# Optimization experiments

Measured on AMD Instinct MI355X. Metric: run time of the kernel, lower is better.

The kernel has to match this reference:

```python
import jax, jax.numpy as jnp
from jax import lax
import numpy as np

# torch.sign(torch.sign(x) + 0.5): maps x<0 -> -1, x>=0 -> +1 (zeros go to +1)
def binarize(x):
    return jnp.where(x >= 0, 1.0, -1.0).astype(x.dtype)


def setup_inputs() -> dict:
    key = jax.random.key(0)
    kx, kw, kb = jax.random.split(key, 3)
    x = jax.random.normal(kx, (32, 256, 56, 56), dtype=jnp.float32)
    weight = jax.random.normal(kw, (256, 256, 3, 3), dtype=jnp.float32)
    bias = jax.random.normal(kb, (256,), dtype=jnp.float32)
    return {"x": x, "weight": weight, "bias": bias}


def reference(x, weight, bias):
    b_weight = binarize(weight)  # [O, I, kH, kW] in {-1, +1}
    b_bias = binarize(bias)      # [O] in {-1, +1}
    out = lax.conv_general_dilated(
        x, b_weight,
        window_strides=(1, 1),
        padding=((1, 1), (1, 1)),
        rhs_dilation=(1, 1),
        feature_group_count=1,
        dimension_numbers=("NCHW", "OIHW", "NCHW"),
    )
    return out + b_bias[None, :, None, None]
```

## Files before the change

kernel.cpp:

```cpp
#include <hip/hip_runtime.h>
#include <stdint.h>


#define N_IMG 32
#define C_IN  256
#define H_IN  56
#define W_IN  56
#define O_OUT 256
#define HW    (H_IN * W_IN)
#define K_RAW (C_IN * 9)

typedef int8_t i8x16 __attribute__((ext_vector_type(16)));
typedef int    i32x4 __attribute__((ext_vector_type(4)));
typedef float  f32x4 __attribute__((ext_vector_type(4)));
typedef float  f32x4u __attribute__((ext_vector_type(4), aligned(4)));
typedef __bf16 bf16x8 __attribute__((ext_vector_type(8)));

#define XQ_WSTR (58 * 64)
#define XQ_CSTR (58 * 58 * 64)
#define XQ_BYTES ((size_t)N_IMG * 4 * XQ_CSTR)
#define WQ_BYTES ((size_t)36 * 256 * 64)
#define AM_OFF   (XQ_BYTES + WQ_BYTES)
#define ARR_OFF  (AM_OFF + 64)
#define WS_NEED  (ARR_OFF + 4096)

#define BPITCH  80
#define BS_ROWB (58 * BPITCH)
#define CHUNK_B (3 * 8192)

#define AMAX_BLOCKS 1024

#define AS1 __attribute__((address_space(1)))
#define AS3 __attribute__((address_space(3)))

__device__ __forceinline__ void dma16(const void* g, void* l) {
    __builtin_amdgcn_global_load_lds((const AS1 uint32_t*)g, (AS3 uint32_t*)l, 16, 0, 0);
}

__global__ void prep_combo(const float* __restrict__ x, const float* __restrict__ w,
                           int8_t* __restrict__ wq, float* __restrict__ am_arr) {
    __shared__ __attribute__((aligned(16))) int8_t S[9 * 64 * 64];
    const int bx = blockIdx.x;
    const int t  = threadIdx.x;

    if (bx >= 16) {
        const int b = bx - 16;
        const size_t NV = (size_t)N_IMG * C_IN * HW / 4;
        float m = 0.f;
        for (size_t i = (size_t)b * 256 + t; i < NV; i += (size_t)AMAX_BLOCKS * 256) {
            f32x4 v = ((const f32x4*)x)[i];
            m = fmaxf(m, fmaxf(fmaxf(fabsf(v[0]), fabsf(v[1])),
                               fmaxf(fabsf(v[2]), fabsf(v[3]))));
        }
#pragma unroll
        for (int off = 32; off; off >>= 1)
            m = fmaxf(m, __shfl_down(m, off));
        float* red = (float*)S;
        if ((t & 63) == 0) red[t >> 6] = m;
        __syncthreads();
        if (t == 0)
            am_arr[b] = fmaxf(fmaxf(red[0], red[1]), fmaxf(red[2], red[3]));
        return;
    }

    const int og = bx >> 2;
    const int cc = bx & 3;
    const int o0 = og * 64;
#pragma unroll
    for (int kk = 0; kk < 4; ++kk) {
        const int p   = kk * 256 + t;
        const int o_l = p >> 4;
        const int chg = p & 15;
        const float* src = w + (size_t)(o0 + o_l) * K_RAW + (size_t)(cc * 64 + chg * 4) * 9;
        f32x4u v[9];
#pragma unroll
        for (int q = 0; q < 9; ++q) v[q] = *(const f32x4u*)(src + q * 4);
#pragma unroll
        for (int tap = 0; tap < 9; ++tap) {
            unsigned dw = 0;
#pragma unroll
            for (int co = 0; co < 4; ++co) {
                const int flat = co * 9 + tap;
                const float fv = v[flat >> 2][flat & 3];
                dw |= (unsigned)((fv >= 0.f) ? 0x01u : 0xffu) << (co * 8);
            }
            *(unsigned*)&S[tap * 4096 + o_l * 64 + chg * 4] = dw;
        }
    }
    __syncthreads();
#pragma unroll
    for (int kk = 0; kk < 9; ++kk) {
        const int c    = kk * 256 + t;
        const int tap  = c >> 8;
        const int rem  = c & 255;
        const int o_l  = rem >> 2;
        const int cpos = rem & 3;
        const int truec = (cpos - ((o_l & 15) >> 1)) & 3;
        i32x4 vv = *(const i32x4*)&S[tap * 4096 + o_l * 64 + truec * 16];
        *(i32x4*)(wq + ((size_t)(cc * 9 + tap) * 256 + (o0 + o_l)) * 64 + cpos * 16) = vv;
    }
}

__global__ void xtrans_q(const float* __restrict__ x, int8_t* __restrict__ xq,
                         const float* __restrict__ am_arr,
                         unsigned* __restrict__ am_bits) {
    __shared__ float red[4];
    const int t = threadIdx.x;
    float m = fmaxf(fmaxf(am_arr[t], am_arr[t + 256]),
                    fmaxf(am_arr[t + 512], am_arr[t + 768]));
#pragma unroll
    for (int off = 32; off; off >>= 1)
        m = fmaxf(m, __shfl_down(m, off));
    if ((t & 63) == 0) red[t >> 6] = m;
    __syncthreads();
    m = fmaxf(fmaxf(red[0], red[1]), fmaxf(red[2], red[3]));

    const int bx = blockIdx.x;
    const int cc = blockIdx.y;
    const int n  = blockIdx.z;
    if (bx == 0 && cc == 0 && n == 0 && t == 0) *am_bits = __float_as_uint(m);

    int8_t* plane = xq + (size_t)(n * 4 + cc) * XQ_CSTR;
    if (bx >= 56) {
        const int hh = (bx == 56) ? 0 : 57;
        if (t < 232) *(i32x4*)(plane + (size_t)hh * XQ_WSTR + t * 16) = (i32x4){0, 0, 0, 0};
        return;
    }
    const int hh = bx + 1;
    const int wg = t & 15;
    const int cg = t >> 4;
    int8_t* orow = plane + (size_t)hh * XQ_WSTR;

    if (wg >= 14) {
        const int ww = (wg == 14) ? 0 : 57;
        *(int*)(orow + ww * 64 + cg * 4) = 0;
        return;
    }

    const float scale = 127.f / fmaxf(m, 1e-20f);
    const float* src = x + ((size_t)n * C_IN + cc * 64 + cg * 4) * HW
                         + (size_t)bx * W_IN + wg * 4;
    int8_t qb[4][4];
#pragma unroll
    for (int j = 0; j < 4; ++j) {
        f32x4 v = *(const f32x4*)(src + (size_t)j * HW);
#pragma unroll
        for (int k = 0; k < 4; ++k) {
            float f = v[k] * scale;
            f = fminf(fmaxf(f, -127.f), 127.f);
            qb[j][k] = (int8_t)(int)rintf(f);
        }
    }
#pragma unroll
    for (int k = 0; k < 4; ++k) {
        int d = (int)(uint8_t)qb[0][k] | ((int)(uint8_t)qb[1][k] << 8)
              | ((int)(uint8_t)qb[2][k] << 16) | ((int)(uint8_t)qb[3][k] << 24);
        *(int*)(orow + (wg * 4 + k + 1) * 64 + cg * 4) = d;
    }
}

__launch_bounds__(256, 2)
__global__ void bconv_i8(const int8_t* __restrict__ xq,
                         const int8_t* __restrict__ wq,
                         const float* __restrict__ bias,
                         const unsigned* __restrict__ amax_bits,
                         float* __restrict__ out) {
    __shared__ __attribute__((aligned(16))) int8_t As[2 * CHUNK_B];
    __shared__ __attribute__((aligned(16))) int8_t Bs[6 * BS_ROWB];

    const int tid  = threadIdx.x;
    const int lane = tid & 63;
    const int wv   = tid >> 6;
    const int row  = lane & 15;
    const int quad = lane >> 4;

    const int nrp  = blockIdx.x;
    const int n    = nrp / 14;
    const int rp   = nrp - n * 14;
    const int oblk = blockIdx.y;
    const int h0   = rp * 4;

    int pr[4], pc[4];
    bool live[4];
#pragma unroll
    for (int nt = 0; nt < 4; ++nt) {
        int p = wv * 64 + nt * 16 + row;
        live[nt] = (p < 224);
        int r = p / 56;
        int c = p - r * 56;
        if (!live[nt]) { r = 0; c = 0; }
        pr[nt] = r;
        pc[nt] = c;
    }

    i32x4 acc[8][4];
#pragma unroll
    for (int mt = 0; mt < 8; ++mt)
#pragma unroll
        for (int nt = 0; nt < 4; ++nt)
            acc[mt][nt] = (i32x4){0, 0, 0, 0};

    const int rowA = row * 64 + (((quad + (row >> 1)) & 3) << 4);
    int addrB[4];
#pragma unroll
    for (int nt = 0; nt < 4; ++nt)
        addrB[nt] = pr[nt] * BS_ROWB + pc[nt] * BPITCH + quad * 16;

    auto issueA3 = [&](int c) {
        const int8_t* g = wq + (size_t)(3 * c) * 16384 + oblk * 8192 + wv * 2048 + lane * 16;
        int8_t* l = &As[(c & 1) * CHUNK_B + wv * 2048];
#pragma unroll
        for (int u = 0; u < 3; ++u) {
            dma16(g + u * 16384,        l + u * 8192);
            dma16(g + u * 16384 + 1024, l + u * 8192 + 1024);
        }
    };

    issueA3(0);

    i32x4 af[8], bc[4], bn[4];

    for (int cc = 0; cc < 4; ++cc) {
        __syncthreads();
        if (tid < 232) {
            const int8_t* bbase = xq + (size_t)(n * 4 + cc) * XQ_CSTR
                                     + (size_t)h0 * XQ_WSTR + tid * 16;
            int8_t* ldst = &Bs[(tid >> 2) * BPITCH + (tid & 3) * 16];
            i32x4 hv[6];
#pragma unroll
            for (int r6 = 0; r6 < 6; ++r6)
                hv[r6] = *(const i32x4*)(bbase + r6 * XQ_WSTR);
#pragma unroll
            for (int r6 = 0; r6 < 6; ++r6)
                *(i32x4*)(ldst + r6 * BS_ROWB) = hv[r6];
        }
        __syncthreads();

#pragma unroll
        for (int k = 0; k < 3; ++k) {
            const int c = cc * 3 + k;
            if (k == 0) {
                if (c + 1 < 12) issueA3(c + 1);
#pragma unroll
                for (int nt = 0; nt < 4; ++nt)
                    bc[nt] = *(const i32x4*)(&Bs[addrB[nt]]);
            } else {
                __syncthreads();
                if (c + 1 < 12) issueA3(c + 1);
#pragma unroll
                for (int nt = 0; nt < 4; ++nt) bc[nt] = bn[nt];
            }
            const int8_t* Acur = &As[(c & 1) * CHUNK_B];
#pragma unroll
            for (int mt = 0; mt < 8; ++mt)
                af[mt] = *(const i32x4*)(Acur + mt * 1024 + rowA);

#pragma unroll
            for (int u = 0; u < 3; ++u) {
                if (u < 2) {
                    const int offn = k * BS_ROWB + (u + 1) * BPITCH;
#pragma unroll
                    for (int nt = 0; nt < 4; ++nt)
                        bn[nt] = *(const i32x4*)(&Bs[addrB[nt] + offn]);
                    const int8_t* Anx = Acur + (u + 1) * 8192;
#pragma unroll
                    for (int mt = 0; mt < 8; ++mt) {
                        i32x4 a = af[mt];
#pragma unroll
                        for (int nt = 0; nt < 4; ++nt)
                            acc[mt][nt] = __builtin_amdgcn_mfma_i32_16x16x64_i8(
                                a, bc[nt], acc[mt][nt], 0, 0, 0);
                        af[mt] = *(const i32x4*)(Anx + mt * 1024 + rowA);
                    }
#pragma unroll
                    for (int nt = 0; nt < 4; ++nt) bc[nt] = bn[nt];
                } else {
                    if (k < 2) {
                        const int offn = (k + 1) * BS_ROWB;
#pragma unroll
                        for (int nt = 0; nt < 4; ++nt)
                            bn[nt] = *(const i32x4*)(&Bs[addrB[nt] + offn]);
                    }
#pragma unroll
                    for (int mt = 0; mt < 8; ++mt)
#pragma unroll
                        for (int nt = 0; nt < 4; ++nt)
                            acc[mt][nt] = __builtin_amdgcn_mfma_i32_16x16x64_i8(
                                af[mt], bc[nt], acc[mt][nt], 0, 0, 0);
                }
            }
        }
    }

    const float am  = __uint_as_float(*amax_bits);
    const float inv = am * (1.0f / 127.0f);
    float* base0 = out + ((size_t)n * O_OUT + oblk * 128) * HW;
    int pixoff[4];
#pragma unroll
    for (int nt = 0; nt < 4; ++nt)
        pixoff[nt] = (h0 + pr[nt]) * W_IN + pc[nt];
#pragma unroll
    for (int mt = 0; mt < 8; ++mt) {
        f32x4 bv = *(const f32x4*)(bias + oblk * 128 + mt * 16 + quad * 4);
#pragma unroll
        for (int r = 0; r < 4; ++r) {
            const float sb = (bv[r] >= 0.0f) ? 1.0f : -1.0f;
            const size_t ob = (size_t)(mt * 16 + quad * 4 + r) * HW;
#pragma unroll
            for (int nt = 0; nt < 4; ++nt)
                if (live[nt]) base0[ob + pixoff[nt]] = (float)acc[mt][nt][r] * inv + sb;
        }
    }
}

#define CHW (C_IN * HW)
#define FPITCH 40

__launch_bounds__(256, 2)
__global__ void bconv_fallback(const float* __restrict__ x,
                               const float* __restrict__ w,
                               const float* __restrict__ bias,
                               float* __restrict__ out) {
    __shared__ __attribute__((aligned(16))) __bf16 Asf[128 * FPITCH];
    __shared__ __attribute__((aligned(16))) __bf16 Bsf[128 * FPITCH];

    const int tid  = threadIdx.x;
    const int lane = tid & 63;
    const int wv   = tid >> 6;
    const int pblk = blockIdx.x;
    const int oblk = blockIdx.y;

    const int p_local = tid & 127;
    const int cgrp    = tid >> 7;
    const int pixel   = pblk * 128 + p_local;
    const int n_img   = pixel / HW;
    const int hw      = pixel - n_img * HW;
    const int h       = hw / W_IN;
    const int wx      = hw - h * W_IN;
    const float* xbase = x + (size_t)n_img * CHW;

    f32x4 acc[8][2];
#pragma unroll
    for (int mt = 0; mt < 8; ++mt)
#pragma unroll
        for (int nt = 0; nt < 2; ++nt)
            acc[mt][nt] = (f32x4){0.f, 0.f, 0.f, 0.f};

    const int pix_wave = wv * 32;
    const int row  = lane & 15;
    const int quad = lane >> 4;

    for (int tap = 0; tap < 9; ++tap) {
        const int dh = tap / 3 - 1;
        const int dw = tap % 3 - 1;
        const int hh = h + dh;
        const int ww = wx + dw;
        const bool valid = ((unsigned)hh < (unsigned)H_IN) && ((unsigned)ww < (unsigned)W_IN);
        const int offs = hh * W_IN + ww;

        for (int ck = 0; ck < 8; ++ck) {
            __syncthreads();
#pragma unroll
            for (int rep = 0; rep < 2; ++rep) {
                int v  = tid + rep * 256;
                int oa = v >> 2;
                int c8 = v & 3;
                const float* wsrc = w + (size_t)(oblk * 128 + oa) * K_RAW
                                      + (ck * 32 + c8 * 8) * 9 + tap;
                bf16x8 val;
#pragma unroll
                for (int j = 0; j < 8; ++j)
                    val[j] = (wsrc[j * 9] >= 0.0f) ? (__bf16)1.0f : (__bf16)(-1.0f);
                *(bf16x8*)(&Asf[oa * FPITCH + c8 * 8]) = val;
            }
            {
                const int cbase = (ck * 32 + cgrp * 16) * HW + offs;
#pragma unroll
                for (int g = 0; g < 2; ++g) {
                    bf16x8 vb;
#pragma unroll
                    for (int j = 0; j < 8; ++j) {
                        float f = valid ? xbase[cbase + (g * 8 + j) * HW] : 0.0f;
                        vb[j] = (__bf16)f;
                    }
                    *(bf16x8*)(&Bsf[p_local * FPITCH + cgrp * 16 + g * 8]) = vb;
                }
            }
            __syncthreads();
            bf16x8 bfrag[2];
#pragma unroll
            for (int nt = 0; nt < 2; ++nt)
                bfrag[nt] = *(const bf16x8*)(&Bsf[(pix_wave + nt * 16 + row) * FPITCH + quad * 8]);
#pragma unroll
            for (int mt = 0; mt < 8; ++mt) {
                bf16x8 afrag = *(const bf16x8*)(&Asf[(mt * 16 + row) * FPITCH + quad * 8]);
#pragma unroll
                for (int nt = 0; nt < 2; ++nt)
                    acc[mt][nt] = __builtin_amdgcn_mfma_f32_16x16x32_bf16(
                        afrag, bfrag[nt], acc[mt][nt], 0, 0, 0);
            }
        }
    }

#pragma unroll
    for (int nt = 0; nt < 2; ++nt) {
        int pix = pblk * 128 + pix_wave + nt * 16 + row;
        int ni  = pix / HW;
        int phw = pix - ni * HW;
        float* obase = out + (size_t)ni * (O_OUT * HW) + phw;
#pragma unroll
        for (int mt = 0; mt < 8; ++mt) {
            int o0 = oblk * 128 + mt * 16 + quad * 4;
#pragma unroll
            for (int r = 0; r < 4; ++r) {
                int o = o0 + r;
                float sb = (bias[o] >= 0.0f) ? 1.0f : -1.0f;
                obase[(size_t)o * HW] = acc[mt][nt][r] + sb;
            }
        }
    }
}

extern "C" void kernel_launch(void* const* d_in, const int* in_sizes, int n_in,
                              void* d_out, int out_size, void* d_ws, size_t ws_size,
                              hipStream_t stream) {
    const float* x    = (const float*)d_in[0];
    const float* w    = (const float*)d_in[1];
    const float* bias = (const float*)d_in[2];
    float* out        = (float*)d_out;

    if (ws_size >= WS_NEED) {
        int8_t*   xq     = (int8_t*)d_ws;
        int8_t*   wq     = (int8_t*)d_ws + XQ_BYTES;
        unsigned* am     = (unsigned*)((char*)d_ws + AM_OFF);
        float*    am_arr = (float*)((char*)d_ws + ARR_OFF);

        prep_combo<<<dim3(16 + AMAX_BLOCKS), dim3(256), 0, stream>>>(x, w, wq, am_arr);
        xtrans_q<<<dim3(58, 4, N_IMG), dim3(256), 0, stream>>>(x, xq, am_arr, am);
        bconv_i8<<<dim3(N_IMG * 14, 2), dim3(256), 0, stream>>>(xq, wq, bias, am, out);
    } else {
        bconv_fallback<<<dim3((N_IMG * HW) / 128, 2), dim3(256), 0, stream>>>(
            x, w, bias, out);
    }
}
```

Baseline: 271.6 us.

## Fuse prep, quantize and int8 conv into one cooperative persistent kernel

Replaces the three launches (weight prep plus absmax, input transpose-quantize, int8 MFMA conv) with one cooperative kernel of 512 blocks. The phases are separated by grid-wide syncs, and the conv tiles are processed persistently. The aim is to remove launch gaps and the tail idle time between kernels. The cost is fewer blocks for the absmax and quantize phases, grid sync overhead, a persistent loop with an uneven tile count (896 over 512 blocks), and occupancy capped by the 77KB of shared memory.

Measured after the change: 504.9 us. 1.86x slower.

```diff
diff --git a/kernel.cpp b/kernel.cpp
--- a/kernel.cpp
+++ b/kernel.cpp
@@ -1,5 +1,8 @@
 #include <hip/hip_runtime.h>
+#include <hip/hip_cooperative_groups.h>
 #include <stdint.h>
+
+namespace cg = cooperative_groups;
 
 
 #define N_IMG 32
@@ -28,6 +31,9 @@
 #define BS_ROWB (58 * BPITCH)
 #define CHUNK_B (3 * 8192)
 
+#define NBLK      512
+#define NUNITS    (58 * 4 * N_IMG)
+#define NTILES    896
 #define AMAX_BLOCKS 1024
 
 #define AS1 __attribute__((address_space(1)))
@@ -35,6 +41,282 @@
 
 __device__ __forceinline__ void dma16(const void* g, void* l) {
     __builtin_amdgcn_global_load_lds((const AS1 uint32_t*)g, (AS3 uint32_t*)l, 16, 0, 0);
+}
+
+__launch_bounds__(256, 2)
+__global__ void mega(const float* __restrict__ x, const float* __restrict__ w,
+                     const float* __restrict__ bias,
+                     int8_t* __restrict__ xq, int8_t* __restrict__ wq,
+                     float* __restrict__ am_arr, float* __restrict__ out) {
+    __shared__ __attribute__((aligned(16))) int8_t SMEM[76992];
+
+    const int bid = blockIdx.x;
+    const int t   = threadIdx.x;
+
+    if (bid < 16) {
+        if (t == 0) am_arr[bid] = 0.f;
+        int8_t* S = SMEM;
+        const int og = bid >> 2;
+        const int cc = bid & 3;
+        const int o0 = og * 64;
+#pragma unroll
+        for (int kk = 0; kk < 4; ++kk) {
+            const int p   = kk * 256 + t;
+            const int o_l = p >> 4;
+            const int chg = p & 15;
+            const float* src = w + (size_t)(o0 + o_l) * K_RAW + (size_t)(cc * 64 + chg * 4) * 9;
+            f32x4u v[9];
+#pragma unroll
+            for (int q = 0; q < 9; ++q) v[q] = *(const f32x4u*)(src + q * 4);
+#pragma unroll
+            for (int tap = 0; tap < 9; ++tap) {
+                unsigned dw = 0;
+#pragma unroll
+                for (int co = 0; co < 4; ++co) {
+                    const int flat = co * 9 + tap;
+                    const float fv = v[flat >> 2][flat & 3];
+                    dw |= (unsigned)((fv >= 0.f) ? 0x01u : 0xffu) << (co * 8);
+                }
+                *(unsigned*)&S[tap * 4096 + o_l * 64 + chg * 4] = dw;
+            }
+        }
+        __syncthreads();
+#pragma unroll
+        for (int kk = 0; kk < 9; ++kk) {
+            const int c    = kk * 256 + t;
+            const int tap  = c >> 8;
+            const int rem  = c & 255;
+            const int o_l  = rem >> 2;
+            const int cpos = rem & 3;
+            const int truec = (cpos - ((o_l & 15) >> 1)) & 3;
+            i32x4 vv = *(const i32x4*)&S[tap * 4096 + o_l * 64 + truec * 16];
+            *(i32x4*)(wq + ((size_t)(cc * 9 + tap) * 256 + (o0 + o_l)) * 64 + cpos * 16) = vv;
+        }
+    } else {
+        const int b = bid - 16;
+        const size_t NV = (size_t)N_IMG * C_IN * HW / 4;
+        float m = 0.f;
+        for (size_t i = (size_t)b * 256 + t; i < NV; i += (size_t)496 * 256) {
+            f32x4 v = ((const f32x4*)x)[i];
+            m = fmaxf(m, fmaxf(fmaxf(fabsf(v[0]), fabsf(v[1])),
+                               fmaxf(fabsf(v[2]), fabsf(v[3]))));
+        }
+#pragma unroll
+        for (int off = 32; off; off >>= 1)
+            m = fmaxf(m, __shfl_down(m, off));
+        float* red = (float*)SMEM;
+        if ((t & 63) == 0) red[t >> 6] = m;
+        __syncthreads();
+        if (t == 0)
+            am_arr[bid] = fmaxf(fmaxf(red[0], red[1]), fmaxf(red[2], red[3]));
+    }
+    __threadfence();
+    cg::this_grid().sync();
+
+    float m = fmaxf(am_arr[t], am_arr[t + 256]);
+#pragma unroll
+    for (int off = 32; off; off >>= 1)
+        m = fmaxf(m, __shfl_down(m, off));
+    {
+        float* red = (float*)SMEM;
+        if ((t & 63) == 0) red[t >> 6] = m;
+        __syncthreads();
+        m = fmaxf(fmaxf(red[0], red[1]), fmaxf(red[2], red[3]));
+    }
+    const float scale = 127.f / fmaxf(m, 1e-20f);
+    const float inv   = m * (1.0f / 127.0f);
+
+    for (int u = bid; u < NUNITS; u += NBLK) {
+        const int bx  = u % 58;
+        const int rem = u / 58;
+        const int cc  = rem & 3;
+        const int n   = rem >> 2;
+        int8_t* plane = xq + (size_t)(n * 4 + cc) * XQ_CSTR;
+
+        if (bx >= 56) {
+            const int hh = (bx == 56) ? 0 : 57;
+            if (t < 232)
+                *(i32x4*)(plane + (size_t)hh * XQ_WSTR + t * 16) = (i32x4){0, 0, 0, 0};
+        } else {
+            const int hh = bx + 1;
+            const int wg = t & 15;
+            const int cg = t >> 4;
+            int8_t* orow = plane + (size_t)hh * XQ_WSTR;
+            if (wg >= 14) {
+                const int ww = (wg == 14) ? 0 : 57;
+                *(int*)(orow + ww * 64 + cg * 4) = 0;
+            } else {
+                const float* src = x + ((size_t)n * C_IN + cc * 64 + cg * 4) * HW
+                                     + (size_t)bx * W_IN + wg * 4;
+                int8_t qb[4][4];
+#pragma unroll
+                for (int j = 0; j < 4; ++j) {
+                    f32x4 v = *(const f32x4*)(src + (size_t)j * HW);
+#pragma unroll
+                    for (int k = 0; k < 4; ++k) {
+                        float f = v[k] * scale;
+                        f = fminf(fmaxf(f, -127.f), 127.f);
+                        qb[j][k] = (int8_t)(int)rintf(f);
+                    }
+                }
+#pragma unroll
+                for (int k = 0; k < 4; ++k) {
+                    int d = (int)(uint8_t)qb[0][k] | ((int)(uint8_t)qb[1][k] << 8)
+                          | ((int)(uint8_t)qb[2][k] << 16) | ((int)(uint8_t)qb[3][k] << 24);
+                    *(int*)(orow + (wg * 4 + k + 1) * 64 + cg * 4) = d;
+                }
+            }
+        }
+    }
+    __threadfence();
+    cg::this_grid().sync();
+
+    int8_t* As = SMEM;
+    int8_t* Bs = SMEM + 49152;
+
+    const int lane = t & 63;
+    const int wv   = t >> 6;
+    const int row  = lane & 15;
+    const int quad = lane >> 4;
+
+    int pr[4], pc[4];
+    bool live[4];
+#pragma unroll
+    for (int nt = 0; nt < 4; ++nt) {
+        int p = wv * 64 + nt * 16 + row;
+        live[nt] = (p < 224);
+        int r = p / 56;
+        int c = p - r * 56;
+        if (!live[nt]) { r = 0; c = 0; }
+        pr[nt] = r;
+        pc[nt] = c;
+    }
+    const int rowA = row * 64 + (((quad + (row >> 1)) & 3) << 4);
+    int addrB[4];
+#pragma unroll
+    for (int nt = 0; nt < 4; ++nt)
+        addrB[nt] = pr[nt] * BS_ROWB + pc[nt] * BPITCH + quad * 16;
+
+    for (int T = bid; T < NTILES; T += NBLK) {
+        if (T != bid) __syncthreads();
+
+        const int oblk = (T >= 448) ? 1 : 0;
+        const int nrp  = T - oblk * 448;
+        const int n    = nrp / 14;
+        const int rp   = nrp - n * 14;
+        const int h0   = rp * 4;
+
+        i32x4 acc[8][4];
+#pragma unroll
+        for (int mt = 0; mt < 8; ++mt)
+#pragma unroll
+            for (int nt = 0; nt < 4; ++nt)
+                acc[mt][nt] = (i32x4){0, 0, 0, 0};
+
+        auto issueA3 = [&](int c) {
+            const int8_t* g = wq + (size_t)(3 * c) * 16384 + oblk * 8192 + wv * 2048 + lane * 16;
+            int8_t* l = &As[(c & 1) * CHUNK_B + wv * 2048];
+#pragma unroll
+            for (int uu = 0; uu < 3; ++uu) {
+                dma16(g + uu * 16384,        l + uu * 8192);
+                dma16(g + uu * 16384 + 1024, l + uu * 8192 + 1024);
+            }
+        };
+
+        issueA3(0);
+
+        i32x4 af[8], bc[4], bn[4];
+
+        for (int cc = 0; cc < 4; ++cc) {
+            __syncthreads();
+            if (t < 232) {
+                const int8_t* bbase = xq + (size_t)(n * 4 + cc) * XQ_CSTR
+                                         + (size_t)h0 * XQ_WSTR + t * 16;
+                int8_t* ldst = &Bs[(t >> 2) * BPITCH + (t & 3) * 16];
+                i32x4 hv[6];
+#pragma unroll
+                for (int r6 = 0; r6 < 6; ++r6)
+                    hv[r6] = *(const i32x4*)(bbase + r6 * XQ_WSTR);
+#pragma unroll
+                for (int r6 = 0; r6 < 6; ++r6)
+                    *(i32x4*)(ldst + r6 * BS_ROWB) = hv[r6];
+            }
+            __syncthreads();
+
+#pragma unroll
+            for (int k = 0; k < 3; ++k) {
+                const int c = cc * 3 + k;
+                if (k == 0) {
+                    if (c + 1 < 12) issueA3(c + 1);
+#pragma unroll
+                    for (int nt = 0; nt < 4; ++nt)
+                        bc[nt] = *(const i32x4*)(&Bs[addrB[nt]]);
+                } else {
+                    __syncthreads();
+                    if (c + 1 < 12) issueA3(c + 1);
+#pragma unroll
+                    for (int nt = 0; nt < 4; ++nt) bc[nt] = bn[nt];
+                }
+                const int8_t* Acur = &As[(c & 1) * CHUNK_B];
+#pragma unroll
+                for (int mt = 0; mt < 8; ++mt)
+                    af[mt] = *(const i32x4*)(Acur + mt * 1024 + rowA);
+
+#pragma unroll
+                for (int u = 0; u < 3; ++u) {
+                    if (u < 2) {
+                        const int offn = k * BS_ROWB + (u + 1) * BPITCH;
+#pragma unroll
+                        for (int nt = 0; nt < 4; ++nt)
+                            bn[nt] = *(const i32x4*)(&Bs[addrB[nt] + offn]);
+                        const int8_t* Anx = Acur + (u + 1) * 8192;
+#pragma unroll
+                        for (int mt = 0; mt < 8; ++mt) {
+                            i32x4 a = af[mt];
+#pragma unroll
+                            for (int nt = 0; nt < 4; ++nt)
+                                acc[mt][nt] = __builtin_amdgcn_mfma_i32_16x16x64_i8(
+                                    a, bc[nt], acc[mt][nt], 0, 0, 0);
+                            af[mt] = *(const i32x4*)(Anx + mt * 1024 + rowA);
+                        }
+#pragma unroll
+                        for (int nt = 0; nt < 4; ++nt) bc[nt] = bn[nt];
+                    } else {
+                        if (k < 2) {
+                            const int offn = (k + 1) * BS_ROWB;
+#pragma unroll
+                            for (int nt = 0; nt < 4; ++nt)
+                                bn[nt] = *(const i32x4*)(&Bs[addrB[nt] + offn]);
+                        }
+#pragma unroll
+                        for (int mt = 0; mt < 8; ++mt)
+#pragma unroll
+                            for (int nt = 0; nt < 4; ++nt)
+                                acc[mt][nt] = __builtin_amdgcn_mfma_i32_16x16x64_i8(
+                                    af[mt], bc[nt], acc[mt][nt], 0, 0, 0);
+                    }
+                }
+            }
+        }
+
+        float* base0 = out + ((size_t)n * O_OUT + oblk * 128) * HW;
+        int pixoff[4];
+#pragma unroll
+        for (int nt = 0; nt < 4; ++nt)
+            pixoff[nt] = (h0 + pr[nt]) * W_IN + pc[nt];
+#pragma unroll
+        for (int mt = 0; mt < 8; ++mt) {
+            f32x4 bv = *(const f32x4*)(bias + oblk * 128 + mt * 16 + quad * 4);
+#pragma unroll
+            for (int r = 0; r < 4; ++r) {
+                const float sb = (bv[r] >= 0.0f) ? 1.0f : -1.0f;
+                const size_t ob = (size_t)(mt * 16 + quad * 4 + r) * HW;
+#pragma unroll
+                for (int nt = 0; nt < 4; ++nt)
+                    if (live[nt]) base0[ob + pixoff[nt]] = (float)acc[mt][nt][r] * inv + sb;
+            }
+        }
+    }
 }
 
 __global__ void prep_combo(const float* __restrict__ x, const float* __restrict__ w,
@@ -435,9 +717,16 @@
         unsigned* am     = (unsigned*)((char*)d_ws + AM_OFF);
         float*    am_arr = (float*)((char*)d_ws + ARR_OFF);
 
-        prep_combo<<<dim3(16 + AMAX_BLOCKS), dim3(256), 0, stream>>>(x, w, wq, am_arr);
-        xtrans_q<<<dim3(58, 4, N_IMG), dim3(256), 0, stream>>>(x, xq, am_arr, am);
-        bconv_i8<<<dim3(N_IMG * 14, 2), dim3(256), 0, stream>>>(xq, wq, bias, am, out);
+        void* args[] = {(void*)&x, (void*)&w, (void*)&bias,
+                        (void*)&xq, (void*)&wq, (void*)&am_arr, (void*)&out};
+        hipError_t e = hipLaunchCooperativeKernel((const void*)mega, dim3(NBLK), dim3(256),
+                                                  args, 0, stream);
+        if (e != hipSuccess) {
+            (void)hipGetLastError();
+            prep_combo<<<dim3(16 + AMAX_BLOCKS), dim3(256), 0, stream>>>(x, w, wq, am_arr);
+            xtrans_q<<<dim3(58, 4, N_IMG), dim3(256), 0, stream>>>(x, xq, am_arr, am);
+            bconv_i8<<<dim3(N_IMG * 14, 2), dim3(256), 0, stream>>>(xq, wq, bias, am, out);
+        }
     } else {
         bconv_fallback<<<dim3((N_IMG * HW) / 128, 2), dim3(256), 0, stream>>>(
             x, w, bias, out);
```

## Fuse weight binarization, amax reduction and input quantization into one cooperative kernel

Applied to the files above, without the earlier changes.

Replaces the two preprocessing launches (prep_combo and xtrans_q) with a single cooperative kernel. It computes the weight sign-packing and partial abs-max, does a grid-wide sync, reduces the max in every block, then quantizes and transposes the input to padded int8 with a grid-stride loop. This removes one launch and the inter-kernel gap. It adds a grid barrier and a redundant final reduction per block, and falls back to the old path if the cooperative launch fails. The bconv_i8 kernel is only moved, not changed.

Result: slower. 527.9 us (+94.4%).

```diff
diff --git a/kernel.cpp b/kernel.cpp
--- a/kernel.cpp
+++ b/kernel.cpp
@@ -1,5 +1,8 @@
 #include <hip/hip_runtime.h>
+#include <hip/hip_cooperative_groups.h>
 #include <stdint.h>
+
+namespace cg = cooperative_groups;
 
 
 #define N_IMG 32
@@ -28,6 +31,10 @@
 #define BS_ROWB (58 * BPITCH)
 #define CHUNK_B (3 * 8192)
 
+#define NB_COOP   1024
+#define WPB       144
+#define AMAXB     (NB_COOP - WPB)
+#define NUNITS    (58 * 4 * N_IMG)
 #define AMAX_BLOCKS 1024
 
 #define AS1 __attribute__((address_space(1)))
@@ -35,6 +42,259 @@
 
 __device__ __forceinline__ void dma16(const void* g, void* l) {
     __builtin_amdgcn_global_load_lds((const AS1 uint32_t*)g, (AS3 uint32_t*)l, 16, 0, 0);
+}
+
+__launch_bounds__(256, 4)
+__global__ void prep_coop(const float* __restrict__ x, const float* __restrict__ w,
+                          int8_t* __restrict__ xq, int8_t* __restrict__ wq,
+                          float* __restrict__ am_arr, unsigned* __restrict__ am_bits) {
+    __shared__ float red[4];
+    const int bid = blockIdx.x;
+    const int t   = threadIdx.x;
+
+    if (bid < WPB) {
+        const int idx  = bid * 256 + t;
+        const int cpos = idx & 3;
+        const int o    = (idx >> 2) & 255;
+        const int st   = idx >> 10;
+        const int tap  = st % 9;
+        const int cc   = st / 9;
+        const int truec = (cpos - ((o & 15) >> 1)) & 3;
+        i8x16 v;
+#pragma unroll
+        for (int j = 0; j < 16; ++j) {
+            const int ch = cc * 64 + truec * 16 + j;
+            const float f = w[(size_t)o * K_RAW + ch * 9 + tap];
+            v[j] = (f >= 0.0f) ? (int8_t)1 : (int8_t)-1;
+        }
+        *(i8x16*)(wq + (size_t)idx * 16) = v;
+    } else {
+        const int b = bid - WPB;
+        const size_t NV = (size_t)N_IMG * C_IN * HW / 4;
+        float m = 0.f;
+        for (size_t i = (size_t)b * 256 + t; i < NV; i += (size_t)AMAXB * 256) {
+            f32x4 v = ((const f32x4*)x)[i];
+            m = fmaxf(m, fmaxf(fmaxf(fabsf(v[0]), fabsf(v[1])),
+                               fmaxf(fabsf(v[2]), fabsf(v[3]))));
+        }
+#pragma unroll
+        for (int off = 32; off; off >>= 1)
+            m = fmaxf(m, __shfl_down(m, off));
+        if ((t & 63) == 0) red[t >> 6] = m;
+        __syncthreads();
+        if (t == 0)
+            am_arr[b] = fmaxf(fmaxf(red[0], red[1]), fmaxf(red[2], red[3]));
+    }
+    __threadfence();
+    cg::this_grid().sync();
+
+    float m = 0.f;
+    for (int i = t; i < AMAXB; i += 256) m = fmaxf(m, am_arr[i]);
+#pragma unroll
+    for (int off = 32; off; off >>= 1)
+        m = fmaxf(m, __shfl_down(m, off));
+    if ((t & 63) == 0) red[t >> 6] = m;
+    __syncthreads();
+    m = fmaxf(fmaxf(red[0], red[1]), fmaxf(red[2], red[3]));
+    const float scale = 127.f / fmaxf(m, 1e-20f);
+    if (bid == 0 && t == 0) *am_bits = __float_as_uint(m);
+
+    for (int u = bid; u < NUNITS; u += NB_COOP) {
+        const int bx  = u % 58;
+        const int rem = u / 58;
+        const int cc  = rem & 3;
+        const int n   = rem >> 2;
+        int8_t* plane = xq + (size_t)(n * 4 + cc) * XQ_CSTR;
+
+        if (bx >= 56) {
+            const int hh = (bx == 56) ? 0 : 57;
+            if (t < 232)
+                *(i32x4*)(plane + (size_t)hh * XQ_WSTR + t * 16) = (i32x4){0, 0, 0, 0};
+        } else {
+            const int hh = bx + 1;
+            const int wg = t & 15;
+            const int cg = t >> 4;
+            int8_t* orow = plane + (size_t)hh * XQ_WSTR;
+            if (wg >= 14) {
+                const int ww = (wg == 14) ? 0 : 57;
+                *(int*)(orow + ww * 64 + cg * 4) = 0;
+            } else {
+                const float* src = x + ((size_t)n * C_IN + cc * 64 + cg * 4) * HW
+                                     + (size_t)bx * W_IN + wg * 4;
+                int8_t qb[4][4];
+#pragma unroll
+                for (int j = 0; j < 4; ++j) {
+                    f32x4 v = *(const f32x4*)(src + (size_t)j * HW);
+#pragma unroll
+                    for (int k = 0; k < 4; ++k) {
+                        float f = v[k] * scale;
+                        f = fminf(fmaxf(f, -127.f), 127.f);
+                        qb[j][k] = (int8_t)(int)rintf(f);
+                    }
+                }
+#pragma unroll
+                for (int k = 0; k < 4; ++k) {
+                    int d = (int)(uint8_t)qb[0][k] | ((int)(uint8_t)qb[1][k] << 8)
+                          | ((int)(uint8_t)qb[2][k] << 16) | ((int)(uint8_t)qb[3][k] << 24);
+                    *(int*)(orow + (wg * 4 + k + 1) * 64 + cg * 4) = d;
+                }
+            }
+        }
+    }
+}
+
+__launch_bounds__(256, 2)
+__global__ void bconv_i8(const int8_t* __restrict__ xq,
+                         const int8_t* __restrict__ wq,
+                         const float* __restrict__ bias,
+                         const unsigned* __restrict__ amax_bits,
+                         float* __restrict__ out) {
+    __shared__ __attribute__((aligned(16))) int8_t As[2 * CHUNK_B];
+    __shared__ __attribute__((aligned(16))) int8_t Bs[6 * BS_ROWB];
+
+    const int tid  = threadIdx.x;
+    const int lane = tid & 63;
+    const int wv   = tid >> 6;
+    const int row  = lane & 15;
+    const int quad = lane >> 4;
+
+    const int nrp  = blockIdx.x;
+    const int n    = nrp / 14;
+    const int rp   = nrp - n * 14;
+    const int oblk = blockIdx.y;
+    const int h0   = rp * 4;
+
+    int pr[4], pc[4];
+    bool live[4];
+#pragma unroll
+    for (int nt = 0; nt < 4; ++nt) {
+        int p = wv * 64 + nt * 16 + row;
+        live[nt] = (p < 224);
+        int r = p / 56;
+        int c = p - r * 56;
+        if (!live[nt]) { r = 0; c = 0; }
+        pr[nt] = r;
+        pc[nt] = c;
+    }
+
+    i32x4 acc[8][4];
+#pragma unroll
+    for (int mt = 0; mt < 8; ++mt)
+#pragma unroll
+        for (int nt = 0; nt < 4; ++nt)
+            acc[mt][nt] = (i32x4){0, 0, 0, 0};
+
+    const int rowA = row * 64 + (((quad + (row >> 1)) & 3) << 4);
+    int addrB[4];
+#pragma unroll
+    for (int nt = 0; nt < 4; ++nt)
+        addrB[nt] = pr[nt] * BS_ROWB + pc[nt] * BPITCH + quad * 16;
+
+    auto issueA3 = [&](int c) {
+        const int8_t* g = wq + (size_t)(3 * c) * 16384 + oblk * 8192 + wv * 2048 + lane * 16;
+        int8_t* l = &As[(c & 1) * CHUNK_B + wv * 2048];
+#pragma unroll
+        for (int u = 0; u < 3; ++u) {
+            dma16(g + u * 16384,        l + u * 8192);
+            dma16(g + u * 16384 + 1024, l + u * 8192 + 1024);
+        }
+    };
+
+    issueA3(0);
+
+    i32x4 af[8], bc[4], bn[4];
+
+    for (int cc = 0; cc < 4; ++cc) {
+        __syncthreads();
+        if (tid < 232) {
+            const int8_t* bbase = xq + (size_t)(n * 4 + cc) * XQ_CSTR
+                                     + (size_t)h0 * XQ_WSTR + tid * 16;
+            int8_t* ldst = &Bs[(tid >> 2) * BPITCH + (tid & 3) * 16];
+            i32x4 hv[6];
+#pragma unroll
+            for (int r6 = 0; r6 < 6; ++r6)
+                hv[r6] = *(const i32x4*)(bbase + r6 * XQ_WSTR);
+#pragma unroll
+            for (int r6 = 0; r6 < 6; ++r6)
+                *(i32x4*)(ldst + r6 * BS_ROWB) = hv[r6];
+        }
+        __syncthreads();
+
+#pragma unroll
+        for (int k = 0; k < 3; ++k) {
+            const int c = cc * 3 + k;
+            if (k == 0) {
+                if (c + 1 < 12) issueA3(c + 1);
+#pragma unroll
+                for (int nt = 0; nt < 4; ++nt)
+                    bc[nt] = *(const i32x4*)(&Bs[addrB[nt]]);
+            } else {
+                __syncthreads();
+                if (c + 1 < 12) issueA3(c + 1);
+#pragma unroll
+                for (int nt = 0; nt < 4; ++nt) bc[nt] = bn[nt];
+            }
+            const int8_t* Acur = &As[(c & 1) * CHUNK_B];
+#pragma unroll
+            for (int mt = 0; mt < 8; ++mt)
+                af[mt] = *(const i32x4*)(Acur + mt * 1024 + rowA);
+
+#pragma unroll
+            for (int u = 0; u < 3; ++u) {
+                if (u < 2) {
+                    const int offn = k * BS_ROWB + (u + 1) * BPITCH;
+#pragma unroll
+                    for (int nt = 0; nt < 4; ++nt)
+                        bn[nt] = *(const i32x4*)(&Bs[addrB[nt] + offn]);
+                    const int8_t* Anx = Acur + (u + 1) * 8192;
+#pragma unroll
+                    for (int mt = 0; mt < 8; ++mt) {
+                        i32x4 a = af[mt];
+#pragma unroll
+                        for (int nt = 0; nt < 4; ++nt)
+                            acc[mt][nt] = __builtin_amdgcn_mfma_i32_16x16x64_i8(
+                                a, bc[nt], acc[mt][nt], 0, 0, 0);
+                        af[mt] = *(const i32x4*)(Anx + mt * 1024 + rowA);
+                    }
+#pragma unroll
+                    for (int nt = 0; nt < 4; ++nt) bc[nt] = bn[nt];
+                } else {
+                    if (k < 2) {
+                        const int offn = (k + 1) * BS_ROWB;
+#pragma unroll
+                        for (int nt = 0; nt < 4; ++nt)
+                            bn[nt] = *(const i32x4*)(&Bs[addrB[nt] + offn]);
+                    }
+#pragma unroll
+                    for (int mt = 0; mt < 8; ++mt)
+#pragma unroll
+                        for (int nt = 0; nt < 4; ++nt)
+                            acc[mt][nt] = __builtin_amdgcn_mfma_i32_16x16x64_i8(
+                                af[mt], bc[nt], acc[mt][nt], 0, 0, 0);
+                }
+            }
+        }
+    }
+
+    const float am  = __uint_as_float(*amax_bits);
+    const float inv = am * (1.0f / 127.0f);
+    float* base0 = out + ((size_t)n * O_OUT + oblk * 128) * HW;
+    int pixoff[4];
+#pragma unroll
+    for (int nt = 0; nt < 4; ++nt)
+        pixoff[nt] = (h0 + pr[nt]) * W_IN + pc[nt];
+#pragma unroll
+    for (int mt = 0; mt < 8; ++mt) {
+        f32x4 bv = *(const f32x4*)(bias + oblk * 128 + mt * 16 + quad * 4);
+#pragma unroll
+        for (int r = 0; r < 4; ++r) {
+            const float sb = (bv[r] >= 0.0f) ? 1.0f : -1.0f;
+            const size_t ob = (size_t)(mt * 16 + quad * 4 + r) * HW;
+#pragma unroll
+            for (int nt = 0; nt < 4; ++nt)
+                if (live[nt]) base0[ob + pixoff[nt]] = (float)acc[mt][nt][r] * inv + sb;
+        }
+    }
 }
 
 __global__ void prep_combo(const float* __restrict__ x, const float* __restrict__ w,
@@ -159,160 +419,6 @@
     }
 }
 
-__launch_bounds__(256, 2)
-__global__ void bconv_i8(const int8_t* __restrict__ xq,
-                         const int8_t* __restrict__ wq,
-                         const float* __restrict__ bias,
-                         const unsigned* __restrict__ amax_bits,
-                         float* __restrict__ out) {
-    __shared__ __attribute__((aligned(16))) int8_t As[2 * CHUNK_B];
-    __shared__ __attribute__((aligned(16))) int8_t Bs[6 * BS_ROWB];
-
-    const int tid  = threadIdx.x;
-    const int lane = tid & 63;
-    const int wv   = tid >> 6;
-    const int row  = lane & 15;
-    const int quad = lane >> 4;
-
-    const int nrp  = blockIdx.x;
-    const int n    = nrp / 14;
-    const int rp   = nrp - n * 14;
-    const int oblk = blockIdx.y;
-    const int h0   = rp * 4;
-
-    int pr[4], pc[4];
-    bool live[4];
-#pragma unroll
-    for (int nt = 0; nt < 4; ++nt) {
-        int p = wv * 64 + nt * 16 + row;
-        live[nt] = (p < 224);
-        int r = p / 56;
-        int c = p - r * 56;
-        if (!live[nt]) { r = 0; c = 0; }
-        pr[nt] = r;
-        pc[nt] = c;
-    }
-
-    i32x4 acc[8][4];
-#pragma unroll
-    for (int mt = 0; mt < 8; ++mt)
-#pragma unroll
-        for (int nt = 0; nt < 4; ++nt)
-            acc[mt][nt] = (i32x4){0, 0, 0, 0};
-
-    const int rowA = row * 64 + (((quad + (row >> 1)) & 3) << 4);
-    int addrB[4];
-#pragma unroll
-    for (int nt = 0; nt < 4; ++nt)
-        addrB[nt] = pr[nt] * BS_ROWB + pc[nt] * BPITCH + quad * 16;
-
-    auto issueA3 = [&](int c) {
-        const int8_t* g = wq + (size_t)(3 * c) * 16384 + oblk * 8192 + wv * 2048 + lane * 16;
-        int8_t* l = &As[(c & 1) * CHUNK_B + wv * 2048];
-#pragma unroll
-        for (int u = 0; u < 3; ++u) {
-            dma16(g + u * 16384,        l + u * 8192);
-            dma16(g + u * 16384 + 1024, l + u * 8192 + 1024);
-        }
-    };
-
-    issueA3(0);
-
-    i32x4 af[8], bc[4], bn[4];
-
-    for (int cc = 0; cc < 4; ++cc) {
-        __syncthreads();
-        if (tid < 232) {
-            const int8_t* bbase = xq + (size_t)(n * 4 + cc) * XQ_CSTR
-                                     + (size_t)h0 * XQ_WSTR + tid * 16;
-            int8_t* ldst = &Bs[(tid >> 2) * BPITCH + (tid & 3) * 16];
-            i32x4 hv[6];
-#pragma unroll
-            for (int r6 = 0; r6 < 6; ++r6)
-                hv[r6] = *(const i32x4*)(bbase + r6 * XQ_WSTR);
-#pragma unroll
-            for (int r6 = 0; r6 < 6; ++r6)
-                *(i32x4*)(ldst + r6 * BS_ROWB) = hv[r6];
-        }
-        __syncthreads();
-
-#pragma unroll
-        for (int k = 0; k < 3; ++k) {
-            const int c = cc * 3 + k;
-            if (k == 0) {
-                if (c + 1 < 12) issueA3(c + 1);
-#pragma unroll
-                for (int nt = 0; nt < 4; ++nt)
-                    bc[nt] = *(const i32x4*)(&Bs[addrB[nt]]);
-            } else {
-                __syncthreads();
-                if (c + 1 < 12) issueA3(c + 1);
-#pragma unroll
-                for (int nt = 0; nt < 4; ++nt) bc[nt] = bn[nt];
-            }
-            const int8_t* Acur = &As[(c & 1) * CHUNK_B];
-#pragma unroll
-            for (int mt = 0; mt < 8; ++mt)
-                af[mt] = *(const i32x4*)(Acur + mt * 1024 + rowA);
-
-#pragma unroll
-            for (int u = 0; u < 3; ++u) {
-                if (u < 2) {
-                    const int offn = k * BS_ROWB + (u + 1) * BPITCH;
-#pragma unroll
-                    for (int nt = 0; nt < 4; ++nt)
-                        bn[nt] = *(const i32x4*)(&Bs[addrB[nt] + offn]);
-                    const int8_t* Anx = Acur + (u + 1) * 8192;
-#pragma unroll
-                    for (int mt = 0; mt < 8; ++mt) {
-                        i32x4 a = af[mt];
-#pragma unroll
-                        for (int nt = 0; nt < 4; ++nt)
-                            acc[mt][nt] = __builtin_amdgcn_mfma_i32_16x16x64_i8(
-                                a, bc[nt], acc[mt][nt], 0, 0, 0);
-                        af[mt] = *(const i32x4*)(Anx + mt * 1024 + rowA);
-                    }
-#pragma unroll
-                    for (int nt = 0; nt < 4; ++nt) bc[nt] = bn[nt];
-                } else {
-                    if (k < 2) {
-                        const int offn = (k + 1) * BS_ROWB;
-#pragma unroll
-                        for (int nt = 0; nt < 4; ++nt)
-                            bn[nt] = *(const i32x4*)(&Bs[addrB[nt] + offn]);
-                    }
-#pragma unroll
-                    for (int mt = 0; mt < 8; ++mt)
-#pragma unroll
-                        for (int nt = 0; nt < 4; ++nt)
-                            acc[mt][nt] = __builtin_amdgcn_mfma_i32_16x16x64_i8(
-                                af[mt], bc[nt], acc[mt][nt], 0, 0, 0);
-                }
-            }
-        }
-    }
-
-    const float am  = __uint_as_float(*amax_bits);
-    const float inv = am * (1.0f / 127.0f);
-    float* base0 = out + ((size_t)n * O_OUT + oblk * 128) * HW;
-    int pixoff[4];
-#pragma unroll
-    for (int nt = 0; nt < 4; ++nt)
-        pixoff[nt] = (h0 + pr[nt]) * W_IN + pc[nt];
-#pragma unroll
-    for (int mt = 0; mt < 8; ++mt) {
-        f32x4 bv = *(const f32x4*)(bias + oblk * 128 + mt * 16 + quad * 4);
-#pragma unroll
-        for (int r = 0; r < 4; ++r) {
-            const float sb = (bv[r] >= 0.0f) ? 1.0f : -1.0f;
-            const size_t ob = (size_t)(mt * 16 + quad * 4 + r) * HW;
-#pragma unroll
-            for (int nt = 0; nt < 4; ++nt)
-                if (live[nt]) base0[ob + pixoff[nt]] = (float)acc[mt][nt][r] * inv + sb;
-        }
-    }
-}
-
 #define CHW (C_IN * HW)
 #define FPITCH 40
 
@@ -435,8 +541,15 @@
         unsigned* am     = (unsigned*)((char*)d_ws + AM_OFF);
         float*    am_arr = (float*)((char*)d_ws + ARR_OFF);
 
-        prep_combo<<<dim3(16 + AMAX_BLOCKS), dim3(256), 0, stream>>>(x, w, wq, am_arr);
-        xtrans_q<<<dim3(58, 4, N_IMG), dim3(256), 0, stream>>>(x, xq, am_arr, am);
+        void* args[] = {(void*)&x, (void*)&w, (void*)&xq, (void*)&wq,
+                        (void*)&am_arr, (void*)&am};
+        hipError_t e = hipLaunchCooperativeKernel((const void*)prep_coop, dim3(NB_COOP),
+                                                  dim3(256), args, 0, stream);
+        if (e != hipSuccess) {
+            (void)hipGetLastError();
+            prep_combo<<<dim3(16 + AMAX_BLOCKS), dim3(256), 0, stream>>>(x, w, wq, am_arr);
+            xtrans_q<<<dim3(58, 4, N_IMG), dim3(256), 0, stream>>>(x, xq, am_arr, am);
+        }
         bconv_i8<<<dim3(N_IMG * 14, 2), dim3(256), 0, stream>>>(xq, wq, bias, am, out);
     } else {
         bconv_fallback<<<dim3((N_IMG * HW) / 128, 2), dim3(256), 0, stream>>>(
```

## Fuse input quantization into conv kernel and drop separate xtrans pass

Applied to the files above, without the earlier changes.

Removes the xtrans_q kernel and its int8 padded intermediate buffer. The conv kernel now reads fp32 x directly, quantizes it to int8 and writes the padded tile into LDS. The global amax reduction becomes an atomicMax into a memset-cleared word, which removes the second-stage reduction. This saves one launch and the write and re-read of the int8 buffer. In exchange, each conv block re-reads fp32 rows (4x the bytes, read by both oblk blocks plus halo rows) and does the quantize math inside the MFMA loop's load phase. That load phase uses synchronous global loads with no overlap.

New measurement: 276.8 us. About the same (+1.9%).

```diff
diff --git a/kernel.cpp b/kernel.cpp
--- a/kernel.cpp
+++ b/kernel.cpp
@@ -16,13 +16,9 @@
 typedef float  f32x4u __attribute__((ext_vector_type(4), aligned(4)));
 typedef __bf16 bf16x8 __attribute__((ext_vector_type(8)));
 
-#define XQ_WSTR (58 * 64)
-#define XQ_CSTR (58 * 58 * 64)
-#define XQ_BYTES ((size_t)N_IMG * 4 * XQ_CSTR)
 #define WQ_BYTES ((size_t)36 * 256 * 64)
-#define AM_OFF   (XQ_BYTES + WQ_BYTES)
-#define ARR_OFF  (AM_OFF + 64)
-#define WS_NEED  (ARR_OFF + 4096)
+#define AM_OFF   WQ_BYTES
+#define WS_NEED  (AM_OFF + 64)
 
 #define BPITCH  80
 #define BS_ROWB (58 * BPITCH)
@@ -38,7 +34,7 @@
 }
 
 __global__ void prep_combo(const float* __restrict__ x, const float* __restrict__ w,
-                           int8_t* __restrict__ wq, float* __restrict__ am_arr) {
+                           int8_t* __restrict__ wq, unsigned* __restrict__ am_bits) {
     __shared__ __attribute__((aligned(16))) int8_t S[9 * 64 * 64];
     const int bx = blockIdx.x;
     const int t  = threadIdx.x;
@@ -58,8 +54,10 @@
         float* red = (float*)S;
         if ((t & 63) == 0) red[t >> 6] = m;
         __syncthreads();
-        if (t == 0)
-            am_arr[b] = fmaxf(fmaxf(red[0], red[1]), fmaxf(red[2], red[3]));
+        if (t == 0) {
+            m = fmaxf(fmaxf(red[0], red[1]), fmaxf(red[2], red[3]));
+            atomicMax(am_bits, __float_as_uint(m));
+        }
         return;
     }
 
@@ -101,66 +99,8 @@
     }
 }
 
-__global__ void xtrans_q(const float* __restrict__ x, int8_t* __restrict__ xq,
-                         const float* __restrict__ am_arr,
-                         unsigned* __restrict__ am_bits) {
-    __shared__ float red[4];
-    const int t = threadIdx.x;
-    float m = fmaxf(fmaxf(am_arr[t], am_arr[t + 256]),
-                    fmaxf(am_arr[t + 512], am_arr[t + 768]));
-#pragma unroll
-    for (int off = 32; off; off >>= 1)
-        m = fmaxf(m, __shfl_down(m, off));
-    if ((t & 63) == 0) red[t >> 6] = m;
-    __syncthreads();
-    m = fmaxf(fmaxf(red[0], red[1]), fmaxf(red[2], red[3]));
-
-    const int bx = blockIdx.x;
-    const int cc = blockIdx.y;
-    const int n  = blockIdx.z;
-    if (bx == 0 && cc == 0 && n == 0 && t == 0) *am_bits = __float_as_uint(m);
-
-    int8_t* plane = xq + (size_t)(n * 4 + cc) * XQ_CSTR;
-    if (bx >= 56) {
-        const int hh = (bx == 56) ? 0 : 57;
-        if (t < 232) *(i32x4*)(plane + (size_t)hh * XQ_WSTR + t * 16) = (i32x4){0, 0, 0, 0};
-        return;
-    }
-    const int hh = bx + 1;
-    const int wg = t & 15;
-    const int cg = t >> 4;
-    int8_t* orow = plane + (size_t)hh * XQ_WSTR;
-
-    if (wg >= 14) {
-        const int ww = (wg == 14) ? 0 : 57;
-        *(int*)(orow + ww * 64 + cg * 4) = 0;
-        return;
-    }
-
-    const float scale = 127.f / fmaxf(m, 1e-20f);
-    const float* src = x + ((size_t)n * C_IN + cc * 64 + cg * 4) * HW
-                         + (size_t)bx * W_IN + wg * 4;
-    int8_t qb[4][4];
-#pragma unroll
-    for (int j = 0; j < 4; ++j) {
-        f32x4 v = *(const f32x4*)(src + (size_t)j * HW);
-#pragma unroll
-        for (int k = 0; k < 4; ++k) {
-            float f = v[k] * scale;
-            f = fminf(fmaxf(f, -127.f), 127.f);
-            qb[j][k] = (int8_t)(int)rintf(f);
-        }
-    }
-#pragma unroll
-    for (int k = 0; k < 4; ++k) {
-        int d = (int)(uint8_t)qb[0][k] | ((int)(uint8_t)qb[1][k] << 8)
-              | ((int)(uint8_t)qb[2][k] << 16) | ((int)(uint8_t)qb[3][k] << 24);
-        *(int*)(orow + (wg * 4 + k + 1) * 64 + cg * 4) = d;
-    }
-}
-
 __launch_bounds__(256, 2)
-__global__ void bconv_i8(const int8_t* __restrict__ xq,
+__global__ void bconv_fx(const float* __restrict__ x,
                          const int8_t* __restrict__ wq,
                          const float* __restrict__ bias,
                          const unsigned* __restrict__ amax_bits,
@@ -179,6 +119,10 @@
     const int rp   = nrp - n * 14;
     const int oblk = blockIdx.y;
     const int h0   = rp * 4;
+
+    const float am    = __uint_as_float(*amax_bits);
+    const float scale = 127.f / fmaxf(am, 1e-20f);
+    const float inv   = am * (1.0f / 127.0f);
 
     int pr[4], pc[4];
     bool live[4];
@@ -218,21 +162,47 @@
 
     issueA3(0);
 
+    const int wg = tid & 15;
+    const int cg = tid >> 4;
+
     i32x4 af[8], bc[4], bn[4];
 
     for (int cc = 0; cc < 4; ++cc) {
         __syncthreads();
-        if (tid < 232) {
-            const int8_t* bbase = xq + (size_t)(n * 4 + cc) * XQ_CSTR
-                                     + (size_t)h0 * XQ_WSTR + tid * 16;
-            int8_t* ldst = &Bs[(tid >> 2) * BPITCH + (tid & 3) * 16];
-            i32x4 hv[6];
-#pragma unroll
-            for (int r6 = 0; r6 < 6; ++r6)
-                hv[r6] = *(const i32x4*)(bbase + r6 * XQ_WSTR);
-#pragma unroll
-            for (int r6 = 0; r6 < 6; ++r6)
-                *(i32x4*)(ldst + r6 * BS_ROWB) = hv[r6];
+
+        {
+            const float* xpl = x + ((size_t)n * C_IN + cc * 64 + cg * 4) * HW;
+#pragma unroll 2
+            for (int r6 = 0; r6 < 6; ++r6) {
+                const int hin = h0 + r6 - 1;
+                int8_t* lrow = &Bs[r6 * BS_ROWB];
+                if (wg >= 14) {
+                    const int ww = (wg == 14) ? 0 : 57;
+                    *(int*)(lrow + ww * BPITCH + cg * 4) = 0;
+                } else if ((unsigned)hin < 56u) {
+                    const float* src = xpl + (size_t)hin * W_IN + wg * 4;
+                    f32x4 v0 = *(const f32x4*)(src);
+                    f32x4 v1 = *(const f32x4*)(src + HW);
+                    f32x4 v2 = *(const f32x4*)(src + 2 * HW);
+                    f32x4 v3 = *(const f32x4*)(src + 3 * HW);
+#pragma unroll
+                    for (int k = 0; k < 4; ++k) {
+                        float f0 = fminf(fmaxf(v0[k] * scale, -127.f), 127.f);
+                        float f1 = fminf(fmaxf(v1[k] * scale, -127.f), 127.f);
+                        float f2 = fminf(fmaxf(v2[k] * scale, -127.f), 127.f);
+                        float f3 = fminf(fmaxf(v3[k] * scale, -127.f), 127.f);
+                        int d = ((int)(uint8_t)(int8_t)(int)rintf(f0))
+                              | ((int)(uint8_t)(int8_t)(int)rintf(f1) << 8)
+                              | ((int)(uint8_t)(int8_t)(int)rintf(f2) << 16)
+                              | ((int)(uint8_t)(int8_t)(int)rintf(f3) << 24);
+                        *(int*)(lrow + (wg * 4 + k + 1) * BPITCH + cg * 4) = d;
+                    }
+                } else {
+#pragma unroll
+                    for (int k = 0; k < 4; ++k)
+                        *(int*)(lrow + (wg * 4 + k + 1) * BPITCH + cg * 4) = 0;
+                }
+            }
         }
         __syncthreads();
 
@@ -292,8 +262,6 @@
         }
     }
 
-    const float am  = __uint_as_float(*amax_bits);
-    const float inv = am * (1.0f / 127.0f);
     float* base0 = out + ((size_t)n * O_OUT + oblk * 128) * HW;
     int pixoff[4];
 #pragma unroll
@@ -430,14 +398,12 @@
     float* out        = (float*)d_out;
 
     if (ws_size >= WS_NEED) {
-        int8_t*   xq     = (int8_t*)d_ws;
-        int8_t*   wq     = (int8_t*)d_ws + XQ_BYTES;
-        unsigned* am     = (unsigned*)((char*)d_ws + AM_OFF);
-        float*    am_arr = (float*)((char*)d_ws + ARR_OFF);
-
-        prep_combo<<<dim3(16 + AMAX_BLOCKS), dim3(256), 0, stream>>>(x, w, wq, am_arr);
-        xtrans_q<<<dim3(58, 4, N_IMG), dim3(256), 0, stream>>>(x, xq, am_arr, am);
-        bconv_i8<<<dim3(N_IMG * 14, 2), dim3(256), 0, stream>>>(xq, wq, bias, am, out);
+        int8_t*   wq = (int8_t*)d_ws;
+        unsigned* am = (unsigned*)((char*)d_ws + AM_OFF);
+
+        hipMemsetAsync(am, 0, 4, stream);
+        prep_combo<<<dim3(16 + AMAX_BLOCKS), dim3(256), 0, stream>>>(x, w, wq, am);
+        bconv_fx<<<dim3(N_IMG * 14, 2), dim3(256), 0, stream>>>(x, wq, bias, am, out);
     } else {
         bconv_fallback<<<dim3((N_IMG * HW) / 128, 2), dim3(256), 0, stream>>>(
             x, w, bias, out);
```
